# Kernel tuning notes

Hardware: AMD Instinct MI355X
Metric: run time of the kernel (lower is better)

Reference implementation:

```python
import jax, jax.numpy as jnp
import numpy as np
from jax import lax

K = 3
K2 = 9
PAD = 1
GN_GROUPS = 32
GN_EPS = 1e-5
COS_EPS = 1e-8


def conv2d(x, w):
    # 3x3, stride 1, pad 1, NCHW/OIHW
    return lax.conv_general_dilated(x, w, (1, 1), ((PAD, PAD), (PAD, PAD)),
                                    dimension_numbers=('NCHW', 'OIHW', 'NCHW'))


def group_norm(x, gamma, beta):
    N, C, H, W = x.shape
    xg = x.reshape(N, GN_GROUPS, C // GN_GROUPS, H, W)
    m = xg.mean(axis=(2, 3, 4), keepdims=True)
    v = xg.var(axis=(2, 3, 4), keepdims=True)
    xn = ((xg - m) * lax.rsqrt(v + GN_EPS)).reshape(N, C, H, W)
    return xn * gamma[None, :, None, None] + beta[None, :, None, None]


def deform_conv(x, offset, weight):
    # mmcv DeformConv, deformable_groups=1: offset [N, 2*K2, H, W] as (dy,dx) per kernel tap.
    N, C, H, W = x.shape
    off = offset.reshape(N, K2, 2, H, W)
    dy, dx = off[:, :, 0], off[:, :, 1]              # [N,K2,H,W]
    ky, kx = jnp.meshgrid(jnp.arange(K), jnp.arange(K), indexing='ij')
    ky = ky.reshape(K2).astype(x.dtype)
    kx = kx.reshape(K2).astype(x.dtype)
    hh = jnp.arange(H, dtype=x.dtype)
    ww = jnp.arange(W, dtype=x.dtype)
    # absolute (fractional) sample positions per output pixel and kernel tap
    py = hh[None, None, :, None] - PAD + ky[None, :, None, None] + dy   # [N,K2,H,W]
    px = ww[None, None, None, :] - PAD + kx[None, :, None, None] + dx
    y0 = jnp.floor(py)
    x0 = jnp.floor(px)
    ay = py - y0
    ax = px - x0
    xf = x.reshape(N, C, H * W)
    sampled = jnp.zeros((N, C, K2, H, W), x.dtype)
    for oy, wy in ((y0, 1.0 - ay), (y0 + 1.0, ay)):
        for ox, wx in ((x0, 1.0 - ax), (x0 + 1.0, ax)):
            valid = (oy >= 0) & (oy <= H - 1) & (ox >= 0) & (ox <= W - 1)
            yi = jnp.clip(oy, 0, H - 1).astype(jnp.int32)
            xi = jnp.clip(ox, 0, W - 1).astype(jnp.int32)
            idx = (yi * W + xi).reshape(N, 1, K2 * H * W)
            v = jnp.take_along_axis(xf, idx, axis=2).reshape(N, C, K2, H, W)
            w = jnp.where(valid, wy * wx, 0.0)[:, None]   # zero padding outside
            sampled = sampled + v * w
    O = weight.shape[0]
    return jnp.einsum('nckhw,ock->nohw', sampled, weight.reshape(O, C, K2))


def cos_sim(a, b):
    num = jnp.sum(a * b, axis=1)
    na = jnp.sqrt(jnp.sum(a * a, axis=1))
    nb = jnp.sqrt(jnp.sum(b * b, axis=1))
    return num / jnp.maximum(na * nb, COS_EPS)   # [N,H,W]


def agg(support, reference, layers):
    f = jnp.concatenate([support, reference], axis=1)
    for ow, ob, dw, gg, gb in layers[:3]:
        off = conv2d(f, ow) + ob[None, :, None, None]
        f = jax.nn.relu(group_norm(deform_conv(f, off, dw), gg, gb))
    ow, ob, dw, gg, gb = layers[3]
    off = conv2d(f, ow) + ob[None, :, None, None]
    return jax.nn.relu(group_norm(deform_conv(support, off, dw), gg, gb))


def setup_inputs() -> dict:
    key = jax.random.key(0)
    ks = jax.random.split(key, 16)
    C_in, C_out, H, W = 512, 256, 96, 96
    rn = lambda k, shape, s: jax.random.normal(k, shape, jnp.float32) * s
    inp = {'datas': jax.random.normal(ks[0], (2, C_out, H, W), jnp.float32)}
    i = 1
    for n in (1, 2, 3):
        inp[f'off{n}_w'] = rn(ks[i], (18, C_in, 3, 3), 0.01); i += 1
        inp[f'off{n}_b'] = jnp.zeros((18,), jnp.float32)
        inp[f'dcn{n}_w'] = rn(ks[i], (C_in, C_in, 3, 3), 0.02); i += 1
        inp[f'gn{n}_g'] = jnp.ones((C_in,), jnp.float32)
        inp[f'gn{n}_b'] = jnp.zeros((C_in,), jnp.float32)
    inp['off4_w'] = rn(ks[i], (18, C_in, 3, 3), 0.01); i += 1
    inp['off4_b'] = jnp.zeros((18,), jnp.float32)
    inp['dcn4_w'] = rn(ks[i], (C_out, C_out, 3, 3), 0.02); i += 1
    inp['gn4_g'] = jnp.ones((C_out,), jnp.float32)
    inp['gn4_b'] = jnp.zeros((C_out,), jnp.float32)
    return inp


def reference(datas, off1_w, off1_b, dcn1_w, gn1_g, gn1_b,
              off2_w, off2_b, dcn2_w, gn2_g, gn2_b,
              off3_w, off3_b, dcn3_w, gn3_g, gn3_b,
              off4_w, off4_b, dcn4_w, gn4_g, gn4_b):
    layers = [(off1_w, off1_b, dcn1_w, gn1_g, gn1_b),
              (off2_w, off2_b, dcn2_w, gn2_g, gn2_b),
              (off3_w, off3_b, dcn3_w, gn3_g, gn3_b),
              (off4_w, off4_b, dcn4_w, gn4_g, gn4_b)]
    support = datas[:1]
    reference_f = datas[1:]
    tt = agg(reference_f, reference_f, layers)   # [1,C_out,H,W]
    ttw = cos_sim(tt, tt)[:, None]               # [1,1,H,W]
    tk = agg(support, reference_f, layers)
    tkw = cos_sim(tt, tk)[:, None]
    w = jax.nn.softmax(jnp.stack([ttw, tkw], axis=0), axis=0)  # [2,1,1,H,W]
    f = jnp.stack([tt, tk], axis=0)                            # [2,1,C,H,W]
    return jnp.sum(w * f, axis=0)
```

## Files before the change

### kernel.cpp

```cpp
#include <hip/hip_runtime.h>
#include <math.h>

#define HW 9216
#define WIDTH 96
#define FSTRIDE (512*HW)
#define RSTRIDE (256*HW)
#define TABSTRIDE (9*HW)
#define PXP 12544
#define FTPROWS 12800

typedef __attribute__((ext_vector_type(8))) short bf16x8;
typedef __attribute__((ext_vector_type(4))) float f32x4;
typedef __attribute__((ext_vector_type(8))) unsigned short u16x8;

__device__ __forceinline__ unsigned short f2bf(float f) {
  unsigned int u = __float_as_uint(f);
  u += 0x7FFFu + ((u >> 16) & 1u);
  return (unsigned short)(u >> 16);
}
__device__ __forceinline__ float bf2f(unsigned short s) {
  return __uint_as_float(((unsigned int)s) << 16);
}

#define GLDS(g, l) __builtin_amdgcn_global_load_lds( \
    (const __attribute__((address_space(1))) unsigned int*)(g), \
    (__attribute__((address_space(3))) unsigned int*)(l), 16, 0, 0)

__global__ void k_zero(unsigned short* p, unsigned int n8) {
  unsigned int i = blockIdx.x * 256 + threadIdx.x;
  if (i < n8) ((u16x8*)p)[i] = (u16x8){0, 0, 0, 0, 0, 0, 0, 0};
}

__global__ void __launch_bounds__(256) k_mkftp_cat(
    const float* __restrict__ lo0, const float* __restrict__ lo1,
    const float* __restrict__ hi, unsigned short* __restrict__ dst,
    int C, int CB) {
  const int b = blockIdx.z;
  const float* lo = b ? lo1 : lo0;
  unsigned short* d = dst + (size_t)b * FTPROWS * C + 128 * C;
  const int px0 = blockIdx.x * 64, c0 = blockIdx.y * 64;
  __shared__ float tile[64][65];
  const int t = threadIdx.x;
#pragma unroll
  for (int rep = 0; rep < 16; ++rep) {
    int idx = rep * 256 + t;
    int cl = idx >> 6, pl = idx & 63;
    int cg = c0 + cl;
    const float* s = (cg < CB) ? (lo + (size_t)cg * HW) : (hi + (size_t)(cg - CB) * HW);
    tile[cl][pl] = s[px0 + pl];
  }
  __syncthreads();
  const int pl = t >> 2, cu = (t & 3) * 16;
  const int px = px0 + pl;
  const int h = px / WIDTH, w = px - h * WIDTH;
  const size_t pxp = (size_t)(h + 1) * 128 + (w + 1);
  u16x8 o0, o1;
#pragma unroll
  for (int j = 0; j < 8; ++j) o0[j] = f2bf(tile[cu + j][pl]);
#pragma unroll
  for (int j = 0; j < 8; ++j) o1[j] = f2bf(tile[cu + 8 + j][pl]);
  unsigned short* p = d + pxp * C + c0 + cu;
  *(u16x8*)p = o0;
  *(u16x8*)(p + 8) = o1;
}

__global__ void __launch_bounds__(256) k_mkftp_gn(
    const unsigned short* __restrict__ yh, const float2* __restrict__ stat,
    const float* __restrict__ gamma, const float* __restrict__ beta,
    unsigned short* __restrict__ dst) {
  const int C = 512;
  const int b = blockIdx.z;
  unsigned short* d = dst + (size_t)b * FTPROWS * C + 128 * C;
  const int px0 = blockIdx.x * 64, c0 = blockIdx.y * 64;
  __shared__ float tile[64][65];
  const int t = threadIdx.x;
#pragma unroll
  for (int rep = 0; rep < 16; ++rep) {
    int idx = rep * 256 + t;
    int cl = idx >> 6, pl = idx & 63;
    int cg = c0 + cl;
    float2 st = stat[b * 32 + (cg >> 4)];
    float v = bf2f(yh[(size_t)b * FSTRIDE + (size_t)cg * HW + px0 + pl]);
    v = (v - st.x) * st.y * gamma[cg] + beta[cg];
    tile[cl][pl] = fmaxf(v, 0.f);
  }
  __syncthreads();
  const int pl = t >> 2, cu = (t & 3) * 16;
  const int px = px0 + pl;
  const int h = px / WIDTH, w = px - h * WIDTH;
  const size_t pxp = (size_t)(h + 1) * 128 + (w + 1);
  u16x8 o0, o1;
#pragma unroll
  for (int j = 0; j < 8; ++j) o0[j] = f2bf(tile[cu + j][pl]);
#pragma unroll
  for (int j = 0; j < 8; ++j) o1[j] = f2bf(tile[cu + 8 + j][pl]);
  unsigned short* p = d + pxp * C + c0 + cu;
  *(u16x8*)p = o0;
  *(u16x8*)(p + 8) = o1;
}

__global__ void k_prepW_all(const float* __restrict__ ow0, const float* __restrict__ ow1,
                            const float* __restrict__ ow2, const float* __restrict__ ow3,
                            unsigned short* __restrict__ wt) {
  int i = blockIdx.x * 256 + threadIdx.x;
  int lyr = i / 147456, r0 = i % 147456;
  const float* ow = (lyr == 0) ? ow0 : (lyr == 1) ? ow1 : (lyr == 2) ? ow2 : ow3;
  int k = r0 / (32 * 512), r = r0 - k * 32 * 512;
  int oc = r / 512, c = r - oc * 512;
  wt[i] = (oc < 18) ? f2bf(ow[((size_t)oc * 512 + c) * 9 + k]) : (unsigned short)0;
}

__global__ void k_prepA_all(const float* __restrict__ dw0, const float* __restrict__ dw1,
                            const float* __restrict__ dw2, const float* __restrict__ dw3,
                            unsigned short* __restrict__ ap) {
  int i = blockIdx.x * 256 + threadIdx.x;
  int lyr, o, C; size_t base;
  if (i < 7077888) { lyr = i / 2359296; o = i % 2359296; C = 512; base = (size_t)lyr * 2359296; }
  else             { lyr = 3; o = i - 7077888; C = 256; base = 7077888; }
  const float* dw = (lyr == 0) ? dw0 : (lyr == 1) ? dw1 : (lyr == 2) ? dw2 : dw3;
  int K = 9 * C;
  int m = o / K, r = o - m * K;
  int k = r / C, c = r - k * C;
  ap[base + o] = f2bf(dw[((size_t)m * C + c) * 9 + k]);
}

__global__ void __launch_bounds__(256) k_offmm(const unsigned short* __restrict__ ftp,
                                               const unsigned short* __restrict__ Wt,
                                               float* __restrict__ part) {
  const int C = 512;
  __shared__ unsigned short As[2][128 * 64];
  __shared__ unsigned short Bs[2][32 * 64];
  const int tid = threadIdx.x;
  const int lane = tid & 63, wv = tid >> 6;

  const int nwg = gridDim.x;
  const int cpx = nwg >> 3;
  const int bid = blockIdx.x;
  const int l = (bid & 7) * cpx + (bid >> 3);
  const int ks = l % 3;
  const int r = l / 3;
  const int pxi = r % 96;
  const int b = r / 96;
  const int pxp0 = 128 + pxi * 128;
  const unsigned short* fb = ftp + (size_t)b * FTPROWS * C + 128 * C;

  const int lr = lane >> 3;
  const int lu = lane & 7;
  const int fr = lane & 15, hi = lane >> 4;

  f32x4 acc[2][2];
#pragma unroll
  for (int i = 0; i < 2; ++i)
#pragma unroll
    for (int j = 0; j < 2; ++j) acc[i][j] = (f32x4){0.f, 0.f, 0.f, 0.f};

#define OFFMM_STAGE(S, BUF)                                                   \
  {                                                                           \
    const int k_ = ks * 3 + ((S) >> 3);                                       \
    const int dlt_ = (k_ / 3 - 1) * 128 + (k_ % 3 - 1);                       \
    const int c0_ = ((S) & 7) * 64;                                           \
    _Pragma("unroll")                                                         \
    for (int q = 0; q < 4; ++q) {                                             \
      int row = wv * 32 + q * 8 + lr;                                         \
      int su = lu ^ (row & 7);                                                \
      GLDS(fb + (size_t)(pxp0 + dlt_ + row) * C + c0_ + su * 8,               \
           (char*)&As[BUF][0] + (wv * 32 + q * 8) * 128);                     \
    }                                                                         \
    {                                                                         \
      int row = wv * 8 + lr;                                                  \
      int su = lu ^ (row & 7);                                                \
      GLDS(Wt + ((size_t)k_ * 32 + row) * C + c0_ + su * 8,                   \
           (char*)&Bs[BUF][0] + wv * 8 * 128);                                \
    }                                                                         \
  }

  OFFMM_STAGE(0, 0);
  for (int s = 0; s < 24; ++s) {
    const int cur = s & 1;
    if (s + 1 < 24) {
      OFFMM_STAGE(s + 1, cur ^ 1);
      asm volatile("s_waitcnt vmcnt(5)" ::: "memory");
    } else {
      asm volatile("s_waitcnt vmcnt(0)" ::: "memory");
    }
    __builtin_amdgcn_s_barrier();
#pragma unroll
    for (int kk = 0; kk < 2; ++kk) {
      bf16x8 a[2], bb[2];
#pragma unroll
      for (int i = 0; i < 2; ++i) {
        int row = wv * 32 + i * 16 + fr;
        a[i] = *(const bf16x8*)&As[cur][row * 64 + (((kk * 4 + hi) ^ (row & 7)) * 8)];
      }
#pragma unroll
      for (int j = 0; j < 2; ++j) {
        int row = j * 16 + fr;
        bb[j] = *(const bf16x8*)&Bs[cur][row * 64 + (((kk * 4 + hi) ^ (row & 7)) * 8)];
      }
#pragma unroll
      for (int i = 0; i < 2; ++i)
#pragma unroll
        for (int j = 0; j < 2; ++j)
          acc[i][j] = __builtin_amdgcn_mfma_f32_16x16x32_bf16(a[i], bb[j], acc[i][j], 0, 0, 0);
    }
    __builtin_amdgcn_s_barrier();
  }

  float* pb = part + ((size_t)(b * 3 + ks)) * PXP * 32;
#pragma unroll
  for (int i = 0; i < 2; ++i)
#pragma unroll
    for (int j = 0; j < 2; ++j) {
      int row0 = pxp0 + wv * 32 + i * 16 + hi * 4;
      int col = j * 16 + fr;
#pragma unroll
      for (int q = 0; q < 4; ++q)
        pb[(size_t)(row0 + q) * 32 + col] = acc[i][j][q];
    }
}

__global__ void k_table(const float* __restrict__ part, const float* __restrict__ ob,
                        int4* __restrict__ tabi, float4* __restrict__ tabw) {
  int b = blockIdx.z, k = blockIdx.y;
  int px = blockIdx.x * 256 + threadIdx.x;
  int h = px / WIDTH, w = px - h * WIDTH;
  size_t pxp = (size_t)(h + 1) * 128 + (w + 1);
  const float* pb = part + (size_t)b * 3 * PXP * 32 + pxp * 32;
  float dy = ob[2 * k] + pb[2 * k] + pb[(size_t)PXP * 32 + 2 * k] + pb[2 * (size_t)PXP * 32 + 2 * k];
  float dx = ob[2 * k + 1] + pb[2 * k + 1] + pb[(size_t)PXP * 32 + 2 * k + 1] + pb[2 * (size_t)PXP * 32 + 2 * k + 1];
  float py = (float)(h - 1 + k / 3) + dy;
  float pxx = (float)(w - 1 + k % 3) + dx;
  float y0 = floorf(py), x0 = floorf(pxx);
  float ay = py - y0, ax = pxx - x0;
  float wy[2] = {1.f - ay, ay}, wx[2] = {1.f - ax, ax};
  int idx[4]; float wt[4];
#pragma unroll
  for (int t = 0; t < 4; ++t) {
    float oy = y0 + (float)(t >> 1);
    float ox = x0 + (float)(t & 1);
    bool valid = (oy >= 0.f) && (oy <= 95.f) && (ox >= 0.f) && (ox <= 95.f);
    int yi = (int)fminf(fmaxf(oy, 0.f), 95.f);
    int xi = (int)fminf(fmaxf(ox, 0.f), 95.f);
    idx[t] = (yi + 1) * 128 + (xi + 1);
    wt[t] = valid ? wy[t >> 1] * wx[t & 1] : 0.f;
  }
  size_t e = (size_t)b * TABSTRIDE + (size_t)k * HW + px;
  tabi[e] = make_int4(idx[0], idx[1], idx[2], idx[3]);
  tabw[e] = make_float4(wt[0], wt[1], wt[2], wt[3]);
}

__global__ void __launch_bounds__(256) k_sample_t(
    const unsigned short* __restrict__ ftp,
    const int4* __restrict__ tabi, const float4* __restrict__ tabw,
    unsigned short* __restrict__ samp, int C, int kbase, int rowK, int yc) {
  const int nwg = gridDim.x;
  const int cpx = nwg >> 3;
  const int bid = blockIdx.x;
  const int l = (bid & 7) * cpx + (bid >> 3);
  const int ci = l % yc;
  const int r = l / yc;
  const int pxi = r % 144;
  const int zk = r / 144;
  const int b = zk & 1, kloc = zk >> 1;
  const int k = kbase + kloc;
  const int t = threadIdx.x;
  const int px = pxi * 64 + (t >> 2);
  const int c = ci * 64 + (t & 3) * 16;
  const unsigned short* fb = ftp + (size_t)b * FTPROWS * C + 128 * C;
  size_t e = (size_t)b * TABSTRIDE + (size_t)k * HW + px;
  int4 id = tabi[e];
  float4 wt = tabw[e];
  float acc[16];
#pragma unroll
  for (int j = 0; j < 16; ++j) acc[j] = 0.f;
  const int ids[4] = {id.x, id.y, id.z, id.w};
  const float wts[4] = {wt.x, wt.y, wt.z, wt.w};
#pragma unroll
  for (int s = 0; s < 4; ++s) {
    const unsigned short* p = fb + (size_t)ids[s] * C + c;
    u16x8 v0 = *(const u16x8*)p;
    u16x8 v1 = *(const u16x8*)(p + 8);
    float wgt = wts[s];
#pragma unroll
    for (int j = 0; j < 8; ++j) acc[j] += wgt * bf2f(v0[j]);
#pragma unroll
    for (int j = 0; j < 8; ++j) acc[8 + j] += wgt * bf2f(v1[j]);
  }
  u16x8 o0, o1;
#pragma unroll
  for (int j = 0; j < 8; ++j) o0[j] = f2bf(acc[j]);
#pragma unroll
  for (int j = 0; j < 8; ++j) o1[j] = f2bf(acc[8 + j]);
  unsigned short* dst = samp + ((size_t)b * HW + px) * rowK + kloc * C + c;
  *(u16x8*)dst = o0;
  *(u16x8*)(dst + 8) = o1;
}

__device__ __forceinline__ void stage_ab96(const unsigned short* __restrict__ Ag,
                                           const unsigned short* __restrict__ Bg,
                                           int lda, int rowK, int kt,
                                           unsigned short* as_, unsigned short* bs_,
                                           int wv, int lane) {
  const int lr = lane >> 2;
  const int lu = lane & 3;
#pragma unroll
  for (int q = 0; q < 2; ++q) {
    int row = wv * 32 + q * 16 + lr;
    int su = lu ^ ((row >> 1) & 3);
    GLDS(Ag + (size_t)row * lda + kt + su * 8, (char*)as_ + (wv * 2 + q) * 1024);
  }
  const int nb = (wv < 2) ? 2 : 1;
  const int bu0 = (wv < 2) ? (2 * wv) : (wv + 2);
  for (int q = 0; q < nb; ++q) {
    int unit = bu0 + q;
    int row = unit * 16 + lr;
    int su = lu ^ ((row >> 1) & 3);
    GLDS(Bg + (size_t)row * rowK + kt + su * 8, (char*)bs_ + unit * 1024);
  }
}

__global__ void __launch_bounds__(256) k_dcgemm(
    const unsigned short* __restrict__ Ap, const unsigned short* __restrict__ Bt,
    unsigned short* __restrict__ Yh, float2* __restrict__ gnp,
    int lda, int rowK, int aOff, int accum, int CperG, int dogn) {
  __shared__ unsigned short As[2][128 * 32];
  __shared__ unsigned short Bs[2][96 * 32];
  const int tid = threadIdx.x;
  const int lane = tid & 63, wv = tid >> 6;

  const int nwg = gridDim.x;
  const int cpx = nwg >> 3;
  const int bid = blockIdx.x;
  const int l = (bid & 7) * cpx + (bid >> 3);
  const int nm = nwg / 192;
  const int m_i = l % nm;
  const int rest = l / nm;
  const int n_i = rest % 96;
  const int b = rest / 96;

  const int m0 = m_i << 7, n0 = n_i * 96;
  const unsigned short* Ag = Ap + (size_t)m0 * lda + aOff;
  const unsigned short* Bg = Bt + ((size_t)b * HW + n0) * rowK;

  const int wm = (wv >> 1) * 64, wn = (wv & 1) * 48;
  const int fr = lane & 15, hi = lane >> 4;
  const int nt = rowK >> 5;

  f32x4 acc[4][3];
#pragma unroll
  for (int i = 0; i < 4; ++i)
#pragma unroll
    for (int j = 0; j < 3; ++j) acc[i][j] = (f32x4){0.f, 0.f, 0.f, 0.f};

  stage_ab96(Ag, Bg, lda, rowK, 0, &As[0][0], &Bs[0][0], wv, lane);

  for (int t = 0; t < nt; ++t) {
    const int cur = t & 1;
    if (t + 1 < nt) {
      stage_ab96(Ag, Bg, lda, rowK, (t + 1) << 5, &As[cur ^ 1][0], &Bs[cur ^ 1][0],
                 wv, lane);
      if (wv < 2) asm volatile("s_waitcnt vmcnt(4)" ::: "memory");
      else        asm volatile("s_waitcnt vmcnt(3)" ::: "memory");
    } else {
      asm volatile("s_waitcnt vmcnt(0)" ::: "memory");
    }
    __builtin_amdgcn_s_barrier();
    __builtin_amdgcn_sched_barrier(0);
    bf16x8 a[4], bb[3];
#pragma unroll
    for (int i = 0; i < 4; ++i) {
      int row = wm + i * 16 + fr;
      a[i] = *(const bf16x8*)&As[cur][row * 32 + ((hi ^ ((row >> 1) & 3)) * 8)];
    }
#pragma unroll
    for (int j = 0; j < 3; ++j) {
      int row = wn + j * 16 + fr;
      bb[j] = *(const bf16x8*)&Bs[cur][row * 32 + ((hi ^ ((row >> 1) & 3)) * 8)];
    }
    __builtin_amdgcn_s_setprio(1);
#pragma unroll
    for (int i = 0; i < 4; ++i)
#pragma unroll
      for (int j = 0; j < 3; ++j)
        acc[i][j] = __builtin_amdgcn_mfma_f32_16x16x32_bf16(a[i], bb[j], acc[i][j], 0, 0, 0);
    __builtin_amdgcn_s_setprio(0);
    __builtin_amdgcn_s_barrier();
  }

  unsigned short* Yb = Yh + (size_t)b * FSTRIDE;
  const int orow = m0 + wm + hi * 4;
  const int ocol = n0 + wn + fr;
  float s_[4], q_[4];
#pragma unroll
  for (int i = 0; i < 4; ++i) { s_[i] = 0.f; q_[i] = 0.f; }
#pragma unroll
  for (int i = 0; i < 4; ++i) {
#pragma unroll
    for (int j = 0; j < 3; ++j) {
      unsigned short* p = Yb + (size_t)(orow + i * 16) * HW + ocol + j * 16;
#pragma unroll
      for (int q = 0; q < 4; ++q) {
        float v = acc[i][j][q];
        if (accum) v += bf2f(p[(size_t)q * HW]);
        p[(size_t)q * HW] = f2bf(v);
        s_[i] += v;
        q_[i] += v * v;
      }
    }
  }

  if (dogn) {
    const int redmax = (CperG == 16) ? 32 : 16;
#pragma unroll
    for (int i = 0; i < 4; ++i) {
      float s = s_[i], q = q_[i];
      for (int off = 1; off <= redmax; off <<= 1) {
        s += __shfl_xor(s, off);
        q += __shfl_xor(q, off);
      }
      int row0 = m0 + wm + i * 16 + ((CperG == 8) ? (lane >> 5) * 8 : 0);
      int g = row0 / CperG;
      bool writer = (CperG == 16) ? (lane == 0) : ((lane & 31) == 0);
      if (writer)
        gnp[(((size_t)(b * 32 + g)) * 96 + n_i) * 2 + (wv & 1)] = make_float2(s, q);
    }
  }
}

__global__ void k_gnfin2(const float2* __restrict__ gnp, float2* __restrict__ stat,
                         int CperG) {
  int t = threadIdx.x;
  float s = 0.f, q = 0.f;
  for (int j = 0; j < 192; ++j) {
    float2 v = gnp[(size_t)t * 192 + j];
    s += v.x; q += v.y;
  }
  float n = (float)(CperG * HW);
  float m = s / n;
  float var = q / n - m * m;
  stat[t] = make_float2(m, rsqrtf(var + 1e-5f));
}

__global__ void __launch_bounds__(256) k_gnstats1h(const unsigned short* __restrict__ yh,
                                                   float2* __restrict__ part, int CperG) {
  const int b = blockIdx.z, g = blockIdx.x, ch = blockIdx.y;
  const int n = CperG * HW;
  const int cs8 = (n >> 4) >> 3;
  const u16x8* p = (const u16x8*)(yh + (size_t)b * FSTRIDE + (size_t)g * n + (size_t)ch * (n >> 4));
  float s = 0.f, q = 0.f;
  for (int i = threadIdx.x; i < cs8; i += 256) {
    u16x8 v = p[i];
#pragma unroll
    for (int j = 0; j < 8; ++j) { float f = bf2f(v[j]); s += f; q += f * f; }
  }
  __shared__ float ss[256], qs[256];
  ss[threadIdx.x] = s; qs[threadIdx.x] = q;
  __syncthreads();
  for (int d = 128; d > 0; d >>= 1) {
    if (threadIdx.x < d) { ss[threadIdx.x] += ss[threadIdx.x + d]; qs[threadIdx.x] += qs[threadIdx.x + d]; }
    __syncthreads();
  }
  if (threadIdx.x == 0) part[((b << 5) + g) * 16 + ch] = make_float2(ss[0], qs[0]);
}

__global__ void k_gnfin(const float2* __restrict__ part, float2* __restrict__ stat,
                        int CperG) {
  int t = threadIdx.x;
  float s = 0.f, q = 0.f;
#pragma unroll
  for (int j = 0; j < 16; ++j) { float2 v = part[t * 16 + j]; s += v.x; q += v.y; }
  float n = (float)(CperG * HW);
  float m = s / n;
  float var = q / n - m * m;
  stat[t] = make_float2(m, rsqrtf(var + 1e-5f));
}

__global__ void __launch_bounds__(256) k_gncos(
    const unsigned short* __restrict__ yh, const float2* __restrict__ stat,
    const float* __restrict__ gamma, const float* __restrict__ beta,
    float* __restrict__ res, float4* __restrict__ cospart) {
  int px = blockIdx.x * 256 + threadIdx.x;
  int cc = blockIdx.y;
  float saa = 0.f, sbb = 0.f, sab = 0.f;
  for (int c = cc * 32; c < cc * 32 + 32; ++c) {
    float2 st0 = stat[c >> 3];
    float2 st1 = stat[32 + (c >> 3)];
    float ga = gamma[c], be = beta[c];
    float a = fmaxf((bf2f(yh[(size_t)c * HW + px]) - st0.x) * st0.y * ga + be, 0.f);
    float b = fmaxf((bf2f(yh[(size_t)FSTRIDE + (size_t)c * HW + px]) - st1.x) * st1.y * ga + be, 0.f);
    res[(size_t)c * HW + px] = a;
    res[(size_t)RSTRIDE + (size_t)c * HW + px] = b;
    saa += a * a; sbb += b * b; sab += a * b;
  }
  cospart[(size_t)cc * HW + px] = make_float4(saa, sbb, sab, 0.f);
}

__global__ void k_cos2(const float4* __restrict__ part, float* __restrict__ wpix) {
  int px = blockIdx.x * 256 + threadIdx.x;
  float saa = 0.f, sbb = 0.f, sab = 0.f;
#pragma unroll
  for (int cc = 0; cc < 8; ++cc) {
    float4 v = part[(size_t)cc * HW + px];
    saa += v.x; sbb += v.y; sab += v.z;
  }
  float na = sqrtf(saa), nb = sqrtf(sbb);
  float ttw = saa / fmaxf(na * na, 1e-8f);
  float tkw = sab / fmaxf(na * nb, 1e-8f);
  float m = fmaxf(ttw, tkw);
  float e0 = expf(ttw - m), e1 = expf(tkw - m);
  wpix[px] = e0 / (e0 + e1);
}

__global__ void k_combine(const float* __restrict__ res, const float* __restrict__ wpix,
                          float* __restrict__ out) {
  int i = blockIdx.x * 256 + threadIdx.x;
  int px = i % HW;
  float w0 = wpix[px];
  out[i] = w0 * res[i] + (1.f - w0) * res[(size_t)RSTRIDE + i];
}

extern "C" void kernel_launch(void* const* d_in, const int* in_sizes, int n_in,
                              void* d_out, int out_size, void* d_ws, size_t ws_size,
                              hipStream_t stream) {
  const float* datas = (const float*)d_in[0];
  const float* ow[4] = {(const float*)d_in[1], (const float*)d_in[6],
                        (const float*)d_in[11], (const float*)d_in[16]};
  const float* ob[4] = {(const float*)d_in[2], (const float*)d_in[7],
                        (const float*)d_in[12], (const float*)d_in[17]};
  const float* dw[4] = {(const float*)d_in[3], (const float*)d_in[8],
                        (const float*)d_in[13], (const float*)d_in[18]};
  const float* gg[4] = {(const float*)d_in[4], (const float*)d_in[9],
                        (const float*)d_in[14], (const float*)d_in[19]};
  const float* gb[4] = {(const float*)d_in[5], (const float*)d_in[10],
                        (const float*)d_in[15], (const float*)d_in[20]};

  const int fullk = (ws_size >= 248500000ull) ? 1 : 0;
  const size_t sampN = fullk ? (2 * (size_t)HW * 4608) : (2 * (size_t)HW * 1536);

  float* ws = (float*)d_ws;
  unsigned short* yh = (unsigned short*)ws;
  float* offp3 = ws + (2 * (size_t)FSTRIDE * 2) / 4;
  float4* tabw = (float4*)(offp3 + 2 * 3 * (size_t)PXP * 32);
  int4*   tabi = (int4*)(tabw + 2 * (size_t)TABSTRIDE);
  float* wpix = (float*)(tabi + 2 * (size_t)TABSTRIDE);
  float2* stat = (float2*)(wpix + HW);
  float2* gnp  = stat + 64;
  float2* gnpart = gnp + 2 * 32 * 96 * 2;
  float4* cospart = (float4*)(gnpart + 1024);
  float* endp = (float*)(cospart + 8 * (size_t)HW);
  size_t ofs = ((size_t)(endp - ws) + 3) & ~(size_t)3;
  unsigned short* samp = (unsigned short*)(ws + ofs);
  unsigned short* apAll = samp + sampN;
  unsigned short* wtAll = apAll + (size_t)7667712;
  unsigned short* ftp512 = wtAll + (size_t)589824;
  unsigned short* ftp256 = fullk ? (samp + 2 * (size_t)HW * 2304)
                                 : (ftp512 + 2 * (size_t)FTPROWS * 512);
  float* res = (float*)(ftp256 + 2 * (size_t)FTPROWS * 256);

  dim3 blk(256);
  k_zero<<<dim3(2 * FTPROWS * 512 / 8 / 256), blk, 0, stream>>>(ftp512, 2u * FTPROWS * 512 / 8);
  k_prepA_all<<<dim3(29952), blk, 0, stream>>>(dw[0], dw[1], dw[2], dw[3], apAll);
  k_prepW_all<<<dim3(2304), blk, 0, stream>>>(ow[0], ow[1], ow[2], ow[3], wtAll);

  for (int lyr = 0; lyr < 4; ++lyr) {
    const int Cx = (lyr < 3) ? 512 : 256;
    const int M  = Cx;
    const int CperG = (lyr < 3) ? 16 : 8;
    const unsigned short* Ap = (lyr < 3) ? (apAll + (size_t)lyr * 2359296)
                                         : (apAll + (size_t)7077888);
    const unsigned short* Wt = wtAll + (size_t)lyr * 147456;
    if (lyr == 0) {
      k_mkftp_cat<<<dim3(144, 8, 2), blk, 0, stream>>>(datas + RSTRIDE, datas,
                                                       datas + RSTRIDE, ftp512, 512, 256);
    } else {
      k_mkftp_gn<<<dim3(144, 8, 2), blk, 0, stream>>>(yh, stat, gg[lyr - 1], gb[lyr - 1],
                                                      ftp512);
    }
    k_offmm<<<dim3(576), blk, 0, stream>>>(ftp512, Wt, offp3);
    k_table<<<dim3(36, 9, 2), blk, 0, stream>>>(offp3, ob[lyr], tabi, tabw);
    const unsigned short* sftp;
    if (lyr < 3) {
      sftp = ftp512;
    } else {
      k_zero<<<dim3(2 * FTPROWS * 256 / 8 / 256), blk, 0, stream>>>(ftp256, 2u * FTPROWS * 256 / 8);
      k_mkftp_cat<<<dim3(144, 4, 2), blk, 0, stream>>>(datas + RSTRIDE, datas,
                                                       datas, ftp256, 256, 256);
      sftp = ftp256;
    }
    const int nch = fullk ? 1 : 3;
    const int nk = 9 / nch;
    const int rowK = nk * Cx;
    const int yc = Cx / 64;
    for (int ch = 0; ch < nch; ++ch) {
      k_sample_t<<<dim3(144 * yc * 2 * nk), blk, 0, stream>>>(sftp, tabi, tabw, samp,
                                                              Cx, ch * nk, rowK, yc);
      k_dcgemm<<<dim3((M / 128) * 96 * 2), blk, 0, stream>>>(
          Ap, samp, yh, gnp, 9 * Cx, rowK, ch * rowK, ch > 0, CperG,
          fullk && (ch == nch - 1));
    }
    if (fullk) {
      k_gnfin2<<<dim3(1), dim3(64), 0, stream>>>(gnp, stat, CperG);
    } else {
      k_gnstats1h<<<dim3(32, 16, 2), blk, 0, stream>>>(yh, gnpart, CperG);
      k_gnfin<<<dim3(1), dim3(64), 0, stream>>>(gnpart, stat, CperG);
    }
  }

  k_gncos<<<dim3(36, 8), blk, 0, stream>>>(yh, stat, gg[3], gb[3], res, cospart);
  k_cos2<<<dim3(36), blk, 0, stream>>>(cospart, wpix);
  k_combine<<<dim3(RSTRIDE / 256), blk, 0, stream>>>(res, wpix, (float*)d_out);
}
```

Measured before the change: 832.8 us.

## Load deform-conv GEMM A operand directly into registers instead of LDS

The weight (A) tiles in the deformable-conv GEMM are now read straight from global memory into per-wave register fragments, with a two-stage register double buffer. B tiles are still staged through LDS, and the loop is unrolled by two with adjusted vmcnt waits. This removes the A LDS allocation and the shared-memory round trip, which lowers LDS use and may raise occupancy. The cost is more VGPRs and uncoalesced 16-byte global loads, since waves that share rows now each load A redundantly. The loop also assumes an even tile count.

```diff
diff --git a/kernel.cpp b/kernel.cpp
--- a/kernel.cpp
+++ b/kernel.cpp
@@ -296,19 +296,11 @@
   *(u16x8*)(dst + 8) = o1;
 }
 
-__device__ __forceinline__ void stage_ab96(const unsigned short* __restrict__ Ag,
-                                           const unsigned short* __restrict__ Bg,
-                                           int lda, int rowK, int kt,
-                                           unsigned short* as_, unsigned short* bs_,
-                                           int wv, int lane) {
+__device__ __forceinline__ void stage_b96(const unsigned short* __restrict__ Bg,
+                                          int rowK, int kt,
+                                          unsigned short* bs_, int wv, int lane) {
   const int lr = lane >> 2;
   const int lu = lane & 3;
-#pragma unroll
-  for (int q = 0; q < 2; ++q) {
-    int row = wv * 32 + q * 16 + lr;
-    int su = lu ^ ((row >> 1) & 3);
-    GLDS(Ag + (size_t)row * lda + kt + su * 8, (char*)as_ + (wv * 2 + q) * 1024);
-  }
   const int nb = (wv < 2) ? 2 : 1;
   const int bu0 = (wv < 2) ? (2 * wv) : (wv + 2);
   for (int q = 0; q < nb; ++q) {
@@ -323,7 +315,6 @@
     const unsigned short* __restrict__ Ap, const unsigned short* __restrict__ Bt,
     unsigned short* __restrict__ Yh, float2* __restrict__ gnp,
     int lda, int rowK, int aOff, int accum, int CperG, int dogn) {
-  __shared__ unsigned short As[2][128 * 32];
   __shared__ unsigned short Bs[2][96 * 32];
   const int tid = threadIdx.x;
   const int lane = tid & 63, wv = tid >> 6;
@@ -352,38 +343,56 @@
 #pragma unroll
     for (int j = 0; j < 3; ++j) acc[i][j] = (f32x4){0.f, 0.f, 0.f, 0.f};
 
-  stage_ab96(Ag, Bg, lda, rowK, 0, &As[0][0], &Bs[0][0], wv, lane);
-
-  for (int t = 0; t < nt; ++t) {
-    const int cur = t & 1;
-    if (t + 1 < nt) {
-      stage_ab96(Ag, Bg, lda, rowK, (t + 1) << 5, &As[cur ^ 1][0], &Bs[cur ^ 1][0],
-                 wv, lane);
-      if (wv < 2) asm volatile("s_waitcnt vmcnt(4)" ::: "memory");
-      else        asm volatile("s_waitcnt vmcnt(3)" ::: "memory");
+#define LOADA(dst, kt2)                                                       \
+  _Pragma("unroll")                                                           \
+  for (int i = 0; i < 4; ++i) {                                               \
+    int row = wm + i * 16 + fr;                                               \
+    dst[i] = *(const bf16x8*)(Ag + (size_t)row * lda + (kt2) + hi * 8);       \
+  }
+
+#define DCG_MFMA(AF, BUF)                                                     \
+  {                                                                           \
+    bf16x8 bb[3];                                                             \
+    _Pragma("unroll")                                                         \
+    for (int j = 0; j < 3; ++j) {                                             \
+      int row = wn + j * 16 + fr;                                             \
+      bb[j] = *(const bf16x8*)&Bs[BUF][row * 32 + ((hi ^ ((row >> 1) & 3)) * 8)]; \
+    }                                                                         \
+    __builtin_amdgcn_s_setprio(1);                                            \
+    _Pragma("unroll")                                                         \
+    for (int i = 0; i < 4; ++i)                                               \
+      _Pragma("unroll")                                                       \
+      for (int j = 0; j < 3; ++j)                                             \
+        acc[i][j] = __builtin_amdgcn_mfma_f32_16x16x32_bf16(AF[i], bb[j],     \
+                                                            acc[i][j], 0, 0, 0); \
+    __builtin_amdgcn_s_setprio(0);                                            \
+  }
+
+  bf16x8 aA[4], aB[4];
+  stage_b96(Bg, rowK, 0, &Bs[0][0], wv, lane);
+  LOADA(aA, 0);
+
+  for (int t = 0; t < nt; t += 2) {
+    stage_b96(Bg, rowK, (t + 1) << 5, &Bs[1][0], wv, lane);
+    LOADA(aB, (t + 1) << 5);
+    if (wv < 2) asm volatile("s_waitcnt vmcnt(6)" ::: "memory");
+    else        asm volatile("s_waitcnt vmcnt(5)" ::: "memory");
+    __builtin_amdgcn_s_barrier();
+    __builtin_amdgcn_sched_barrier(0);
+    DCG_MFMA(aA, 0);
+    __builtin_amdgcn_s_barrier();
+
+    if (t + 2 < nt) {
+      stage_b96(Bg, rowK, (t + 2) << 5, &Bs[0][0], wv, lane);
+      LOADA(aA, (t + 2) << 5);
+      if (wv < 2) asm volatile("s_waitcnt vmcnt(6)" ::: "memory");
+      else        asm volatile("s_waitcnt vmcnt(5)" ::: "memory");
     } else {
       asm volatile("s_waitcnt vmcnt(0)" ::: "memory");
     }
     __builtin_amdgcn_s_barrier();
     __builtin_amdgcn_sched_barrier(0);
-    bf16x8 a[4], bb[3];
-#pragma unroll
-    for (int i = 0; i < 4; ++i) {
-      int row = wm + i * 16 + fr;
-      a[i] = *(const bf16x8*)&As[cur][row * 32 + ((hi ^ ((row >> 1) & 3)) * 8)];
-    }
-#pragma unroll
-    for (int j = 0; j < 3; ++j) {
-      int row = wn + j * 16 + fr;
-      bb[j] = *(const bf16x8*)&Bs[cur][row * 32 + ((hi ^ ((row >> 1) & 3)) * 8)];
-    }
-    __builtin_amdgcn_s_setprio(1);
-#pragma unroll
-    for (int i = 0; i < 4; ++i)
-#pragma unroll
-      for (int j = 0; j < 3; ++j)
-        acc[i][j] = __builtin_amdgcn_mfma_f32_16x16x32_bf16(a[i], bb[j], acc[i][j], 0, 0, 0);
-    __builtin_amdgcn_s_setprio(0);
+    DCG_MFMA(aB, 1);
     __builtin_amdgcn_s_barrier();
   }
 
```

Result: slower. 1.280 ms (+53.7%).
